# Performance work log

Measured on AMD Instinct MI355X. Metric: run time of the kernel, lower is better.

Reference implementation:

```python
import jax, jax.numpy as jnp
import numpy as np

HEADS = 8
NEG_SLOPE = 0.2  # PyG GATConv default negative_slope


def segment_softmax(logits, seg, num_segments):
    # logits: [E, H], seg: [E] destination ids
    m = jax.ops.segment_max(logits, seg, num_segments=num_segments)
    m = jnp.where(jnp.isfinite(m), m, 0.0)
    e = jnp.exp(logits - jax.lax.stop_gradient(m)[seg])
    s = jax.ops.segment_sum(e, seg, num_segments=num_segments)
    return e / (s[seg] + 1e-16)


def setup_inputs() -> dict:
    key = jax.random.key(0)
    k1, k2, k3, k4, k5, k6 = jax.random.split(key, 6)
    N, F_IN, H, C, E = 50000, 116, HEADS, 32, 800000
    x = jax.random.normal(k1, (N, F_IN), dtype=jnp.float32)
    edge_index = jax.random.randint(k2, (2, E), 0, N, dtype=jnp.int64)
    # Params (glorot-ish scale)
    W = jax.random.normal(k3, (F_IN, H * C), dtype=jnp.float32) * (1.0 / np.sqrt(F_IN))
    att_src = jax.random.normal(k4, (1, H, C), dtype=jnp.float32) * (1.0 / np.sqrt(C))
    att_dst = jax.random.normal(k5, (1, H, C), dtype=jnp.float32) * (1.0 / np.sqrt(C))
    bias = jnp.zeros((C,), dtype=jnp.float32)
    return {"x": x, "edge_index": edge_index, "W": W, "att_src": att_src, "att_dst": att_dst, "bias": bias}


def reference(x, edge_index, W, att_src, att_dst, bias):
    N = x.shape[0]
    H = HEADS
    C = W.shape[1] // H
    # Shared linear transform: [N, H, C]
    xt = (x @ W).reshape(N, H, C)
    alpha_src = jnp.sum(xt * att_src, axis=-1)  # [N, H]
    alpha_dst = jnp.sum(xt * att_dst, axis=-1)  # [N, H]
    # add_self_loops=True (PyG GATConv default)
    loops = jnp.arange(N, dtype=edge_index.dtype)
    src = jnp.concatenate([edge_index[0], loops])
    dst = jnp.concatenate([edge_index[1], loops])
    # Edge-wise attention logits + segment softmax over destination
    alpha = jax.nn.leaky_relu(alpha_src[src] + alpha_dst[dst], negative_slope=NEG_SLOPE)  # [E', H]
    alpha = segment_softmax(alpha, dst, N)
    # Weighted message aggregation
    msg = xt[src] * alpha[:, :, None]  # [E', H, C]
    out = jax.ops.segment_sum(msg, dst, num_segments=N)  # [N, H, C]
    # concat=False -> mean over heads, then bias
    out = out.mean(axis=1) + bias  # [N, C]
    return jax.nn.relu(out)
```

## Files before the change

### kernel.cpp

```cpp
#include <hip/hip_runtime.h>
#include <hip/hip_bf16.h>


#define F_IN 116
#define HC 256
#define NHEAD 8
#define CDIM 32
#define KP 128
#define ROWS_PB 48
#define DSLOT 64
#define ECHUNK 4096

typedef unsigned int uint32;
typedef short short8 __attribute__((ext_vector_type(8)));
typedef float f32x4 __attribute__((ext_vector_type(4)));

__device__ __forceinline__ unsigned short f2bf(float f) {
    uint32 u = __float_as_uint(f);
    u = (u + 0x7FFF + ((u >> 16) & 1)) >> 16;
    return (unsigned short)u;
}

__global__ void init_k(const float* __restrict__ W,
                       const float* __restrict__ att_s,
                       const float* __restrict__ att_d,
                       unsigned short* __restrict__ WbT,
                       unsigned short* __restrict__ WaT,
                       int* __restrict__ cnt, int N) {
    int idx = blockIdx.x * 256 + threadIdx.x;
    for (int i = idx; i < N; i += 144 * 256) cnt[i] = 0;
    if (idx < 32768) {
        int n = idx >> 7, k = idx & 127;
        WbT[idx] = (k < F_IN) ? f2bf(W[k * HC + n]) : (unsigned short)0;
    } else {
        int aid = idx - 32768;
        int col = aid >> 7, k = aid & 127;
        int tile = col >> 4;
        int cc = col & 15;
        int h = cc & 7, part = cc >> 3;
        const float* att = tile ? att_d : att_s;
        float s = 0.f;
        if (k < F_IN) {
            for (int c = 0; c < CDIM; ++c)
                s = fmaf(W[k * HC + h * CDIM + c], att[h * CDIM + c], s);
        }
        unsigned short hi = f2bf(s);
        unsigned short v = hi;
        if (part) {
            float rem = s - __uint_as_float((uint32)hi << 16);
            v = f2bf(rem);
        }
        WaT[col * KP + k] = v;
    }
}

__global__ __launch_bounds__(256) void fuse_k(const float* __restrict__ x,
                                              const unsigned short* __restrict__ WbT,
                                              const unsigned short* __restrict__ WaT,
                                              signed char* __restrict__ xq8,
                                              float* __restrict__ scl,
                                              float* __restrict__ asrc,
                                              float* __restrict__ adst,
                                              int N, int nScatGrp, int Ggemm,
                                              const int* __restrict__ src,
                                              const int* __restrict__ dst,
                                              int* __restrict__ cnt,
                                              unsigned short* __restrict__ csr, int E) {
    const int t = threadIdx.x;
    const int g = blockIdx.x >> 3, r = blockIdx.x & 7;
    const int c = g / 5, p = g - c * 5;

    if (p < 3) {
        const int sg = c * 3 + p;
        if (sg >= nScatGrp) return;
        const int sbid = sg * 8 + r;
        const int slice = sbid & 7;
        const int chunk = sbid >> 3;
        const int SLICE = (N + 7) >> 3;
        const int lo = slice * SLICE;
        const int hi = (lo + SLICE < N) ? lo + SLICE : N;
        const int ebase = chunk * ECHUNK + t * 4;
#pragma unroll
        for (int it = 0; it < ECHUNK / 1024; ++it) {
            int e = ebase + it * 1024;
            if (e < E) {
                int4 d4 = *(const int4*)&dst[e];
                int4 s4 = *(const int4*)&src[e];
                if (d4.x >= lo && d4.x < hi) {
                    int rr = atomicAdd(&cnt[d4.x], 1);
                    if (rr < DSLOT) csr[(d4.x << 6) + rr] = (unsigned short)s4.x;
                }
                if (d4.y >= lo && d4.y < hi) {
                    int rr = atomicAdd(&cnt[d4.y], 1);
                    if (rr < DSLOT) csr[(d4.y << 6) + rr] = (unsigned short)s4.y;
                }
                if (d4.z >= lo && d4.z < hi) {
                    int rr = atomicAdd(&cnt[d4.z], 1);
                    if (rr < DSLOT) csr[(d4.z << 6) + rr] = (unsigned short)s4.z;
                }
                if (d4.w >= lo && d4.w < hi) {
                    int rr = atomicAdd(&cnt[d4.w], 1);
                    if (rr < DSLOT) csr[(d4.w << 6) + rr] = (unsigned short)s4.w;
                }
            }
        }
        return;
    }

    const int gbid = (c * 2 + (p - 3)) * 8 + r;
    if (gbid >= Ggemm) return;

    __shared__ unsigned short xbs[16 * ROWS_PB * 8];
    const int row0 = gbid * ROWS_PB;
    for (int u = t; u < 16 * ROWS_PB; u += 256) {
        const int gg = u / ROWS_PB, rr = u - gg * ROWS_PB;
        const int gr = row0 + rr;
        f32x4 v0 = {0.f, 0.f, 0.f, 0.f}, v1 = {0.f, 0.f, 0.f, 0.f};
        if (gr < N) {
            const f32x4* xp = (const f32x4*)(x + (size_t)gr * F_IN + gg * 8);
            if (gg < 14) { v0 = xp[0]; v1 = xp[1]; }
            else if (gg == 14) { v0 = xp[0]; }
        }
        short8 pk;
        pk[0] = (short)f2bf(v0.x); pk[1] = (short)f2bf(v0.y);
        pk[2] = (short)f2bf(v0.z); pk[3] = (short)f2bf(v0.w);
        pk[4] = (short)f2bf(v1.x); pk[5] = (short)f2bf(v1.y);
        pk[6] = (short)f2bf(v1.z); pk[7] = (short)f2bf(v1.w);
        *(short8*)&xbs[u * 8] = pk;
    }
    __syncthreads();

    const int w = t >> 6, l = t & 63;
    const int q = l >> 4, m = l & 15;
    const int ncol0 = w * 64;

    short8 bfr[4][4];
#pragma unroll
    for (int nt = 0; nt < 4; ++nt)
#pragma unroll
        for (int ks = 0; ks < 4; ++ks)
            bfr[nt][ks] = *(const short8*)&WbT[(size_t)(ncol0 + nt * 16 + m) * KP + ks * 32 + q * 8];

    short8 wa[4];
    if (w < 2) {
#pragma unroll
        for (int ks = 0; ks < 4; ++ks)
            wa[ks] = *(const short8*)&WaT[(size_t)(w * 16 + m) * KP + ks * 32 + q * 8];
    }

    f32x4 acc[3][4];
#pragma unroll
    for (int rt = 0; rt < 3; ++rt)
#pragma unroll
        for (int nt = 0; nt < 4; ++nt) acc[rt][nt] = f32x4{0.f, 0.f, 0.f, 0.f};
    f32x4 acc_a[3];
#pragma unroll
    for (int rt = 0; rt < 3; ++rt) acc_a[rt] = f32x4{0.f, 0.f, 0.f, 0.f};

#pragma unroll
    for (int ks = 0; ks < 4; ++ks) {
        short8 a[3];
#pragma unroll
        for (int rt = 0; rt < 3; ++rt)
            a[rt] = *(const short8*)&xbs[((ks * 4 + q) * ROWS_PB + rt * 16 + m) * 8];
#pragma unroll
        for (int nt = 0; nt < 4; ++nt)
#pragma unroll
            for (int rt = 0; rt < 3; ++rt)
                acc[rt][nt] = __builtin_amdgcn_mfma_f32_16x16x32_bf16(bfr[nt][ks], a[rt], acc[rt][nt], 0, 0, 0);
        if (w < 2) {
#pragma unroll
            for (int rt = 0; rt < 3; ++rt)
                acc_a[rt] = __builtin_amdgcn_mfma_f32_16x16x32_bf16(wa[ks], a[rt], acc_a[rt], 0, 0, 0);
        }
    }

#pragma unroll
    for (int rt = 0; rt < 3; ++rt) {
        const int row = row0 + rt * 16 + m;
        float m0 = 0.f, m1 = 0.f;
#pragma unroll
        for (int rr = 0; rr < 4; ++rr) {
            m0 = fmaxf(m0, fmaxf(fabsf(acc[rt][0][rr]), fabsf(acc[rt][1][rr])));
            m1 = fmaxf(m1, fmaxf(fabsf(acc[rt][2][rr]), fabsf(acc[rt][3][rr])));
        }
        m0 = fmaxf(m0, __shfl_xor(m0, 16, 64));
        m0 = fmaxf(m0, __shfl_xor(m0, 32, 64));
        m1 = fmaxf(m1, __shfl_xor(m1, 16, 64));
        m1 = fmaxf(m1, __shfl_xor(m1, 32, 64));
        m0 = fmaxf(m0, 1e-20f);
        m1 = fmaxf(m1, 1e-20f);
        const float i0 = 127.f / m0, i1 = 127.f / m1;
        if (row < N) {
#pragma unroll
            for (int nt = 0; nt < 4; ++nt) {
                const float iv = (nt < 2) ? i0 : i1;
                uint32 pk = 0;
#pragma unroll
                for (int rr = 0; rr < 4; ++rr) {
                    int qv = __float2int_rn(acc[rt][nt][rr] * iv);
                    qv = (qv > 127) ? 127 : ((qv < -127) ? -127 : qv);
                    pk |= ((uint32)qv & 255u) << (8 * rr);
                }
                *(uint32*)&xq8[(size_t)row * HC + ncol0 + nt * 16 + q * 4] = pk;
            }
            if (q == 0) {
                float2 sc;
                sc.x = m0 * (1.f / 127.f);
                sc.y = m1 * (1.f / 127.f);
                *(float2*)&scl[row * NHEAD + 2 * w] = sc;
            }
        }
    }

    if (w < 2) {
        float* ap = (w == 0) ? asrc : adst;
#pragma unroll
        for (int rt = 0; rt < 3; ++rt) {
            f32x4 s;
#pragma unroll
            for (int rr = 0; rr < 4; ++rr) {
                float v = acc_a[rt][rr];
                s[rr] = v + __shfl_xor(v, 32, 64);
            }
            const int row = row0 + rt * 16 + m;
            if (q < 2 && row < N)
                *(f32x4*)&ap[row * NHEAD + q * 4] = s;
        }
    }
}

__global__ __launch_bounds__(256) void aggregate_k(const signed char* __restrict__ xq8,
                                                   const float* __restrict__ scl,
                                                   const float* __restrict__ asrc,
                                                   const float* __restrict__ adst,
                                                   const int* __restrict__ cnt,
                                                   const unsigned short* __restrict__ csr,
                                                   const float* __restrict__ bias,
                                                   float* __restrict__ out, int N) {
    const int t = threadIdx.x;
    const int lg = t & 31;
    const int base = t & 32;
    const int n = blockIdx.x * 8 + (t >> 5);
    if (n >= N) return;

    const int h_f = lg >> 2;
    const int h_w = lg & 7;
    const int e_w = lg >> 3;

    const int beg = n << 6;
    int d = cnt[n];
    if (d > DSLOT) d = DSLOT;

    const float adst_hw = adst[n * NHEAD + h_w];

    float zs = asrc[n * NHEAD + h_f] + adst[n * NHEAD + h_f];
    zs = (zs > 0.f) ? zs : 0.2f * zs;
    const float wself = __expf(zs);
    const float wselfs = wself * scl[n * NHEAD + h_f];

    uint2 sv = ((const uint2*)(xq8 + (size_t)n * HC))[lg];
    float a0 = wselfs * (float)((int)(sv.x << 24) >> 24);
    float a1 = wselfs * (float)((int)(sv.x << 16) >> 24);
    float a2 = wselfs * (float)((int)(sv.x <<  8) >> 24);
    float a3 = wselfs * (float)((int)sv.x         >> 24);
    float a4 = wselfs * (float)((int)(sv.y << 24) >> 24);
    float a5 = wselfs * (float)((int)(sv.y << 16) >> 24);
    float a6 = wselfs * (float)((int)(sv.y <<  8) >> 24);
    float a7 = wselfs * (float)((int)sv.y         >> 24);
    float wsum = wself;

    const int nfull = d >> 2;
    const int rem = d & 3;
    int pos = beg;
    for (int cch = 0; cch < nfull; ++cch, pos += 4) {
        int s_w = (int)csr[pos + e_w];
        float z = asrc[s_w * NHEAD + h_w] + adst_hw;
        z = (z > 0.f) ? z : 0.2f * z;
        float w_reg = __expf(z);
        float wsc_reg = w_reg * scl[s_w * NHEAD + h_w];
#pragma unroll
        for (int e = 0; e < 4; ++e) {
            int s = __shfl(s_w, base + (e << 3), 64);
            float w  = __shfl(w_reg,  base + (e << 3) + h_f, 64);
            float ws = __shfl(wsc_reg, base + (e << 3) + h_f, 64);
            uint2 v = ((const uint2*)(xq8 + (size_t)s * HC))[lg];
            a0 = fmaf(ws, (float)((int)(v.x << 24) >> 24), a0);
            a1 = fmaf(ws, (float)((int)(v.x << 16) >> 24), a1);
            a2 = fmaf(ws, (float)((int)(v.x <<  8) >> 24), a2);
            a3 = fmaf(ws, (float)((int)v.x         >> 24), a3);
            a4 = fmaf(ws, (float)((int)(v.y << 24) >> 24), a4);
            a5 = fmaf(ws, (float)((int)(v.y << 16) >> 24), a5);
            a6 = fmaf(ws, (float)((int)(v.y <<  8) >> 24), a6);
            a7 = fmaf(ws, (float)((int)v.y         >> 24), a7);
            wsum += w;
        }
    }
    if (rem) {
        int s_w = (e_w < rem) ? (int)csr[pos + e_w] : n;
        float z = asrc[s_w * NHEAD + h_w] + adst_hw;
        z = (z > 0.f) ? z : 0.2f * z;
        float w_reg = __expf(z);
        float wsc_reg = w_reg * scl[s_w * NHEAD + h_w];
        for (int e = 0; e < rem; ++e) {
            int s = __shfl(s_w, base + (e << 3), 64);
            float w  = __shfl(w_reg,  base + (e << 3) + h_f, 64);
            float ws = __shfl(wsc_reg, base + (e << 3) + h_f, 64);
            uint2 v = ((const uint2*)(xq8 + (size_t)s * HC))[lg];
            a0 = fmaf(ws, (float)((int)(v.x << 24) >> 24), a0);
            a1 = fmaf(ws, (float)((int)(v.x << 16) >> 24), a1);
            a2 = fmaf(ws, (float)((int)(v.x <<  8) >> 24), a2);
            a3 = fmaf(ws, (float)((int)v.x         >> 24), a3);
            a4 = fmaf(ws, (float)((int)(v.y << 24) >> 24), a4);
            a5 = fmaf(ws, (float)((int)(v.y << 16) >> 24), a5);
            a6 = fmaf(ws, (float)((int)(v.y <<  8) >> 24), a6);
            a7 = fmaf(ws, (float)((int)v.y         >> 24), a7);
            wsum += w;
        }
    }

    const float inv = 1.f / (wsum + 1e-16f);
    a0 *= inv; a1 *= inv; a2 *= inv; a3 *= inv;
    a4 *= inv; a5 *= inv; a6 *= inv; a7 *= inv;

#pragma unroll
    for (int o = 4; o <= 16; o <<= 1) {
        a0 += __shfl_xor(a0, o, 64);
        a1 += __shfl_xor(a1, o, 64);
        a2 += __shfl_xor(a2, o, 64);
        a3 += __shfl_xor(a3, o, 64);
        a4 += __shfl_xor(a4, o, 64);
        a5 += __shfl_xor(a5, o, 64);
        a6 += __shfl_xor(a6, o, 64);
        a7 += __shfl_xor(a7, o, 64);
    }

    if (lg < 4) {
        const float* bp = bias + 8 * lg;
        float4 r0, r1;
        r0.x = fmaxf(a0 * 0.125f + bp[0], 0.f);
        r0.y = fmaxf(a1 * 0.125f + bp[1], 0.f);
        r0.z = fmaxf(a2 * 0.125f + bp[2], 0.f);
        r0.w = fmaxf(a3 * 0.125f + bp[3], 0.f);
        r1.x = fmaxf(a4 * 0.125f + bp[4], 0.f);
        r1.y = fmaxf(a5 * 0.125f + bp[5], 0.f);
        r1.z = fmaxf(a6 * 0.125f + bp[6], 0.f);
        r1.w = fmaxf(a7 * 0.125f + bp[7], 0.f);
        *(float4*)&out[(size_t)n * CDIM + 8 * lg] = r0;
        *(float4*)&out[(size_t)n * CDIM + 8 * lg + 4] = r1;
    }
}

extern "C" void kernel_launch(void* const* d_in, const int* in_sizes, int n_in,
                              void* d_out, int out_size, void* d_ws, size_t ws_size,
                              hipStream_t stream) {
    const float* x     = (const float*)d_in[0];
    const int*   ei    = (const int*)d_in[1];
    const float* W     = (const float*)d_in[2];
    const float* att_s = (const float*)d_in[3];
    const float* att_d = (const float*)d_in[4];
    const float* bias  = (const float*)d_in[5];
    float* out = (float*)d_out;

    const int N = in_sizes[0] / F_IN;
    const int E = in_sizes[1] / 2;

    signed char* xq8 = (signed char*)d_ws;
    float* scl = (float*)((char*)d_ws + (size_t)N * HC);
    unsigned short* WbT = (unsigned short*)((char*)d_ws + (size_t)2 * N * HC);
    float* asrc = (float*)(WbT + 256 * KP);
    float* adst = asrc + (size_t)N * NHEAD;
    int*   cnt  = (int*)(adst + (size_t)N * NHEAD);
    unsigned short* csr = (unsigned short*)(cnt + N);
    unsigned short* WaT = csr + (size_t)N * DSLOT;

    const int Ggemm = (N + ROWS_PB - 1) / ROWS_PB;
    const int nchunk = (E + ECHUNK - 1) / ECHUNK;
    const int Gscat = nchunk * 8;
    const int nScatGrp = (Gscat + 7) / 8;
    const int nGemmGrp = (Ggemm + 7) / 8;
    const int cS = (nScatGrp + 2) / 3;
    const int cG = (nGemmGrp + 1) / 2;
    const int ncyc = (cS > cG) ? cS : cG;
    const int Gfuse = ncyc * 5 * 8;

    init_k<<<144, 256, 0, stream>>>(W, att_s, att_d, WbT, WaT, cnt, N);
    fuse_k<<<Gfuse, 256, 0, stream>>>(x, WbT, WaT, xq8, scl, asrc, adst,
                                      N, nScatGrp, Ggemm,
                                      ei, ei + E, cnt, csr, E);
    aggregate_k<<<(N + 7) / 8, 256, 0, stream>>>(xq8, scl, asrc, adst, cnt, csr, bias, out, N);
}
```

Measured before the change: 182.4 us.

## Merge init, scatter/GEMM and aggregation into one cooperative persistent kernel

Replaces the three separate kernel launches with a single cooperative kernel whose grid is sized from occupancy and CU count. Stages are separated by grid-wide syncs, and the blocks loop persistently over scatter chunks, GEMM tiles and aggregation node groups. Odd and even blocks alternate the order of scatter and GEMM so the two overlap. This removes launch gaps and the inter-kernel drain, but adds two grid barriers, per-call host queries (occupancy, device properties), and a smaller grid that may reduce latency hiding in the gather-heavy aggregation.

```diff
diff --git a/kernel.cpp b/kernel.cpp
--- a/kernel.cpp
+++ b/kernel.cpp
@@ -1,5 +1,6 @@
 #include <hip/hip_runtime.h>
 #include <hip/hip_bf16.h>
+#include <hip/hip_cooperative_groups.h>
 
 
 #define F_IN 116
@@ -15,339 +16,341 @@
 typedef short short8 __attribute__((ext_vector_type(8)));
 typedef float f32x4 __attribute__((ext_vector_type(4)));
 
+namespace cg = cooperative_groups;
+
 __device__ __forceinline__ unsigned short f2bf(float f) {
     uint32 u = __float_as_uint(f);
     u = (u + 0x7FFF + ((u >> 16) & 1)) >> 16;
     return (unsigned short)u;
 }
 
-__global__ void init_k(const float* __restrict__ W,
-                       const float* __restrict__ att_s,
-                       const float* __restrict__ att_d,
-                       unsigned short* __restrict__ WbT,
-                       unsigned short* __restrict__ WaT,
-                       int* __restrict__ cnt, int N) {
-    int idx = blockIdx.x * 256 + threadIdx.x;
-    for (int i = idx; i < N; i += 144 * 256) cnt[i] = 0;
-    if (idx < 32768) {
-        int n = idx >> 7, k = idx & 127;
-        WbT[idx] = (k < F_IN) ? f2bf(W[k * HC + n]) : (unsigned short)0;
-    } else {
-        int aid = idx - 32768;
-        int col = aid >> 7, k = aid & 127;
-        int tile = col >> 4;
-        int cc = col & 15;
-        int h = cc & 7, part = cc >> 3;
-        const float* att = tile ? att_d : att_s;
-        float s = 0.f;
-        if (k < F_IN) {
-            for (int c = 0; c < CDIM; ++c)
-                s = fmaf(W[k * HC + h * CDIM + c], att[h * CDIM + c], s);
-        }
-        unsigned short hi = f2bf(s);
-        unsigned short v = hi;
-        if (part) {
-            float rem = s - __uint_as_float((uint32)hi << 16);
-            v = f2bf(rem);
-        }
-        WaT[col * KP + k] = v;
+__global__ __launch_bounds__(256) void gat_k(
+        const float* __restrict__ x,
+        const int* __restrict__ src,
+        const int* __restrict__ dst,
+        const float* __restrict__ W,
+        const float* __restrict__ att_s,
+        const float* __restrict__ att_d,
+        const float* __restrict__ bias,
+        unsigned short* __restrict__ WbT,
+        unsigned short* __restrict__ WaT,
+        signed char* __restrict__ xq8,
+        float* __restrict__ scl,
+        float* __restrict__ asrc,
+        float* __restrict__ adst,
+        int* __restrict__ cnt,
+        unsigned short* __restrict__ csr,
+        float* __restrict__ out,
+        int N, int E, int nchunk, int Ggemm, int NG) {
+    const int t = threadIdx.x;
+    const int b = blockIdx.x;
+    const int G = gridDim.x;
+    __shared__ unsigned short xbs[16 * ROWS_PB * 8];
+
+    for (int i = b * 256 + t; i < N; i += G * 256) cnt[i] = 0;
+    for (int idx = b * 256 + t; idx < 36864; idx += G * 256) {
+        if (idx < 32768) {
+            int n = idx >> 7, k = idx & 127;
+            WbT[idx] = (k < F_IN) ? f2bf(W[k * HC + n]) : (unsigned short)0;
+        } else {
+            int aid = idx - 32768;
+            int col = aid >> 7, k = aid & 127;
+            int tile = col >> 4;
+            int cc = col & 15;
+            int h = cc & 7, part = cc >> 3;
+            const float* att = tile ? att_d : att_s;
+            float s = 0.f;
+            if (k < F_IN) {
+                for (int c = 0; c < CDIM; ++c)
+                    s = fmaf(W[k * HC + h * CDIM + c], att[h * CDIM + c], s);
+            }
+            unsigned short hi = f2bf(s);
+            unsigned short v = hi;
+            if (part) {
+                float rem = s - __uint_as_float((uint32)hi << 16);
+                v = f2bf(rem);
+            }
+            WaT[col * KP + k] = v;
+        }
     }
-}
-
-__global__ __launch_bounds__(256) void fuse_k(const float* __restrict__ x,
-                                              const unsigned short* __restrict__ WbT,
-                                              const unsigned short* __restrict__ WaT,
-                                              signed char* __restrict__ xq8,
-                                              float* __restrict__ scl,
-                                              float* __restrict__ asrc,
-                                              float* __restrict__ adst,
-                                              int N, int nScatGrp, int Ggemm,
-                                              const int* __restrict__ src,
-                                              const int* __restrict__ dst,
-                                              int* __restrict__ cnt,
-                                              unsigned short* __restrict__ csr, int E) {
-    const int t = threadIdx.x;
-    const int g = blockIdx.x >> 3, r = blockIdx.x & 7;
-    const int c = g / 5, p = g - c * 5;
-
-    if (p < 3) {
-        const int sg = c * 3 + p;
-        if (sg >= nScatGrp) return;
-        const int sbid = sg * 8 + r;
-        const int slice = sbid & 7;
-        const int chunk = sbid >> 3;
+    cg::this_grid().sync();
+
+    auto do_scatter = [&]() {
+        const int slice = b & 7;
         const int SLICE = (N + 7) >> 3;
         const int lo = slice * SLICE;
         const int hi = (lo + SLICE < N) ? lo + SLICE : N;
-        const int ebase = chunk * ECHUNK + t * 4;
-#pragma unroll
-        for (int it = 0; it < ECHUNK / 1024; ++it) {
-            int e = ebase + it * 1024;
-            if (e < E) {
-                int4 d4 = *(const int4*)&dst[e];
-                int4 s4 = *(const int4*)&src[e];
-                if (d4.x >= lo && d4.x < hi) {
-                    int rr = atomicAdd(&cnt[d4.x], 1);
-                    if (rr < DSLOT) csr[(d4.x << 6) + rr] = (unsigned short)s4.x;
-                }
-                if (d4.y >= lo && d4.y < hi) {
-                    int rr = atomicAdd(&cnt[d4.y], 1);
-                    if (rr < DSLOT) csr[(d4.y << 6) + rr] = (unsigned short)s4.y;
-                }
-                if (d4.z >= lo && d4.z < hi) {
-                    int rr = atomicAdd(&cnt[d4.z], 1);
-                    if (rr < DSLOT) csr[(d4.z << 6) + rr] = (unsigned short)s4.z;
-                }
-                if (d4.w >= lo && d4.w < hi) {
-                    int rr = atomicAdd(&cnt[d4.w], 1);
-                    if (rr < DSLOT) csr[(d4.w << 6) + rr] = (unsigned short)s4.w;
-                }
-            }
-        }
-        return;
-    }
-
-    const int gbid = (c * 2 + (p - 3)) * 8 + r;
-    if (gbid >= Ggemm) return;
-
-    __shared__ unsigned short xbs[16 * ROWS_PB * 8];
-    const int row0 = gbid * ROWS_PB;
-    for (int u = t; u < 16 * ROWS_PB; u += 256) {
-        const int gg = u / ROWS_PB, rr = u - gg * ROWS_PB;
-        const int gr = row0 + rr;
-        f32x4 v0 = {0.f, 0.f, 0.f, 0.f}, v1 = {0.f, 0.f, 0.f, 0.f};
-        if (gr < N) {
-            const f32x4* xp = (const f32x4*)(x + (size_t)gr * F_IN + gg * 8);
-            if (gg < 14) { v0 = xp[0]; v1 = xp[1]; }
-            else if (gg == 14) { v0 = xp[0]; }
-        }
-        short8 pk;
-        pk[0] = (short)f2bf(v0.x); pk[1] = (short)f2bf(v0.y);
-        pk[2] = (short)f2bf(v0.z); pk[3] = (short)f2bf(v0.w);
-        pk[4] = (short)f2bf(v1.x); pk[5] = (short)f2bf(v1.y);
-        pk[6] = (short)f2bf(v1.z); pk[7] = (short)f2bf(v1.w);
-        *(short8*)&xbs[u * 8] = pk;
-    }
-    __syncthreads();
-
-    const int w = t >> 6, l = t & 63;
-    const int q = l >> 4, m = l & 15;
-    const int ncol0 = w * 64;
-
-    short8 bfr[4][4];
-#pragma unroll
-    for (int nt = 0; nt < 4; ++nt)
-#pragma unroll
-        for (int ks = 0; ks < 4; ++ks)
-            bfr[nt][ks] = *(const short8*)&WbT[(size_t)(ncol0 + nt * 16 + m) * KP + ks * 32 + q * 8];
-
-    short8 wa[4];
-    if (w < 2) {
-#pragma unroll
-        for (int ks = 0; ks < 4; ++ks)
-            wa[ks] = *(const short8*)&WaT[(size_t)(w * 16 + m) * KP + ks * 32 + q * 8];
-    }
-
-    f32x4 acc[3][4];
-#pragma unroll
-    for (int rt = 0; rt < 3; ++rt)
-#pragma unroll
-        for (int nt = 0; nt < 4; ++nt) acc[rt][nt] = f32x4{0.f, 0.f, 0.f, 0.f};
-    f32x4 acc_a[3];
-#pragma unroll
-    for (int rt = 0; rt < 3; ++rt) acc_a[rt] = f32x4{0.f, 0.f, 0.f, 0.f};
-
-#pragma unroll
-    for (int ks = 0; ks < 4; ++ks) {
-        short8 a[3];
-#pragma unroll
-        for (int rt = 0; rt < 3; ++rt)
-            a[rt] = *(const short8*)&xbs[((ks * 4 + q) * ROWS_PB + rt * 16 + m) * 8];
-#pragma unroll
-        for (int nt = 0; nt < 4; ++nt)
+        const int Gs = G >> 3;
+        for (int c = b >> 3; c < nchunk; c += Gs) {
+            const int ebase = c * ECHUNK + t * 4;
+#pragma unroll
+            for (int it = 0; it < ECHUNK / 1024; ++it) {
+                int e = ebase + it * 1024;
+                if (e < E) {
+                    int4 d4 = *(const int4*)&dst[e];
+                    int4 s4 = *(const int4*)&src[e];
+                    if (d4.x >= lo && d4.x < hi) {
+                        int rr = atomicAdd(&cnt[d4.x], 1);
+                        if (rr < DSLOT) csr[(d4.x << 6) + rr] = (unsigned short)s4.x;
+                    }
+                    if (d4.y >= lo && d4.y < hi) {
+                        int rr = atomicAdd(&cnt[d4.y], 1);
+                        if (rr < DSLOT) csr[(d4.y << 6) + rr] = (unsigned short)s4.y;
+                    }
+                    if (d4.z >= lo && d4.z < hi) {
+                        int rr = atomicAdd(&cnt[d4.z], 1);
+                        if (rr < DSLOT) csr[(d4.z << 6) + rr] = (unsigned short)s4.z;
+                    }
+                    if (d4.w >= lo && d4.w < hi) {
+                        int rr = atomicAdd(&cnt[d4.w], 1);
+                        if (rr < DSLOT) csr[(d4.w << 6) + rr] = (unsigned short)s4.w;
+                    }
+                }
+            }
+        }
+    };
+
+    auto do_gemm = [&]() {
+        for (int g2 = b; g2 < Ggemm; g2 += G) {
+            __syncthreads();
+            const int row0 = g2 * ROWS_PB;
+            for (int u = t; u < 16 * ROWS_PB; u += 256) {
+                const int gg = u / ROWS_PB, rr = u - gg * ROWS_PB;
+                const int gr = row0 + rr;
+                f32x4 v0 = {0.f, 0.f, 0.f, 0.f}, v1 = {0.f, 0.f, 0.f, 0.f};
+                if (gr < N) {
+                    const f32x4* xp = (const f32x4*)(x + (size_t)gr * F_IN + gg * 8);
+                    if (gg < 14) { v0 = xp[0]; v1 = xp[1]; }
+                    else if (gg == 14) { v0 = xp[0]; }
+                }
+                short8 pk;
+                pk[0] = (short)f2bf(v0.x); pk[1] = (short)f2bf(v0.y);
+                pk[2] = (short)f2bf(v0.z); pk[3] = (short)f2bf(v0.w);
+                pk[4] = (short)f2bf(v1.x); pk[5] = (short)f2bf(v1.y);
+                pk[6] = (short)f2bf(v1.z); pk[7] = (short)f2bf(v1.w);
+                *(short8*)&xbs[u * 8] = pk;
+            }
+            __syncthreads();
+
+            const int w = t >> 6, l = t & 63;
+            const int q = l >> 4, m = l & 15;
+            const int ncol0 = w * 64;
+
+            short8 bfr[4][4];
+#pragma unroll
+            for (int nt = 0; nt < 4; ++nt)
+#pragma unroll
+                for (int ks = 0; ks < 4; ++ks)
+                    bfr[nt][ks] = *(const short8*)&WbT[(size_t)(ncol0 + nt * 16 + m) * KP + ks * 32 + q * 8];
+
+            short8 wa[4];
+            if (w < 2) {
+#pragma unroll
+                for (int ks = 0; ks < 4; ++ks)
+                    wa[ks] = *(const short8*)&WaT[(size_t)(w * 16 + m) * KP + ks * 32 + q * 8];
+            }
+
+            f32x4 acc[3][4];
 #pragma unroll
             for (int rt = 0; rt < 3; ++rt)
-                acc[rt][nt] = __builtin_amdgcn_mfma_f32_16x16x32_bf16(bfr[nt][ks], a[rt], acc[rt][nt], 0, 0, 0);
-        if (w < 2) {
-#pragma unroll
-            for (int rt = 0; rt < 3; ++rt)
-                acc_a[rt] = __builtin_amdgcn_mfma_f32_16x16x32_bf16(wa[ks], a[rt], acc_a[rt], 0, 0, 0);
-        }
-    }
-
-#pragma unroll
-    for (int rt = 0; rt < 3; ++rt) {
-        const int row = row0 + rt * 16 + m;
-        float m0 = 0.f, m1 = 0.f;
-#pragma unroll
-        for (int rr = 0; rr < 4; ++rr) {
-            m0 = fmaxf(m0, fmaxf(fabsf(acc[rt][0][rr]), fabsf(acc[rt][1][rr])));
-            m1 = fmaxf(m1, fmaxf(fabsf(acc[rt][2][rr]), fabsf(acc[rt][3][rr])));
-        }
-        m0 = fmaxf(m0, __shfl_xor(m0, 16, 64));
-        m0 = fmaxf(m0, __shfl_xor(m0, 32, 64));
-        m1 = fmaxf(m1, __shfl_xor(m1, 16, 64));
-        m1 = fmaxf(m1, __shfl_xor(m1, 32, 64));
-        m0 = fmaxf(m0, 1e-20f);
-        m1 = fmaxf(m1, 1e-20f);
-        const float i0 = 127.f / m0, i1 = 127.f / m1;
-        if (row < N) {
-#pragma unroll
-            for (int nt = 0; nt < 4; ++nt) {
-                const float iv = (nt < 2) ? i0 : i1;
-                uint32 pk = 0;
+#pragma unroll
+                for (int nt = 0; nt < 4; ++nt) acc[rt][nt] = f32x4{0.f, 0.f, 0.f, 0.f};
+            f32x4 acc_a[3];
+#pragma unroll
+            for (int rt = 0; rt < 3; ++rt) acc_a[rt] = f32x4{0.f, 0.f, 0.f, 0.f};
+
+#pragma unroll
+            for (int ks = 0; ks < 4; ++ks) {
+                short8 a[3];
+#pragma unroll
+                for (int rt = 0; rt < 3; ++rt)
+                    a[rt] = *(const short8*)&xbs[((ks * 4 + q) * ROWS_PB + rt * 16 + m) * 8];
+#pragma unroll
+                for (int nt = 0; nt < 4; ++nt)
+#pragma unroll
+                    for (int rt = 0; rt < 3; ++rt)
+                        acc[rt][nt] = __builtin_amdgcn_mfma_f32_16x16x32_bf16(bfr[nt][ks], a[rt], acc[rt][nt], 0, 0, 0);
+                if (w < 2) {
+#pragma unroll
+                    for (int rt = 0; rt < 3; ++rt)
+                        acc_a[rt] = __builtin_amdgcn_mfma_f32_16x16x32_bf16(wa[ks], a[rt], acc_a[rt], 0, 0, 0);
+                }
+            }
+
+#pragma unroll
+            for (int rt = 0; rt < 3; ++rt) {
+                const int row = row0 + rt * 16 + m;
+                float m0 = 0.f, m1 = 0.f;
 #pragma unroll
                 for (int rr = 0; rr < 4; ++rr) {
-                    int qv = __float2int_rn(acc[rt][nt][rr] * iv);
-                    qv = (qv > 127) ? 127 : ((qv < -127) ? -127 : qv);
-                    pk |= ((uint32)qv & 255u) << (8 * rr);
-                }
-                *(uint32*)&xq8[(size_t)row * HC + ncol0 + nt * 16 + q * 4] = pk;
-            }
-            if (q == 0) {
-                float2 sc;
-                sc.x = m0 * (1.f / 127.f);
-                sc.y = m1 * (1.f / 127.f);
-                *(float2*)&scl[row * NHEAD + 2 * w] = sc;
-            }
-        }
-    }
-
-    if (w < 2) {
-        float* ap = (w == 0) ? asrc : adst;
-#pragma unroll
-        for (int rt = 0; rt < 3; ++rt) {
-            f32x4 s;
-#pragma unroll
-            for (int rr = 0; rr < 4; ++rr) {
-                float v = acc_a[rt][rr];
-                s[rr] = v + __shfl_xor(v, 32, 64);
-            }
-            const int row = row0 + rt * 16 + m;
-            if (q < 2 && row < N)
-                *(f32x4*)&ap[row * NHEAD + q * 4] = s;
-        }
-    }
-}
-
-__global__ __launch_bounds__(256) void aggregate_k(const signed char* __restrict__ xq8,
-                                                   const float* __restrict__ scl,
-                                                   const float* __restrict__ asrc,
-                                                   const float* __restrict__ adst,
-                                                   const int* __restrict__ cnt,
-                                                   const unsigned short* __restrict__ csr,
-                                                   const float* __restrict__ bias,
-                                                   float* __restrict__ out, int N) {
-    const int t = threadIdx.x;
-    const int lg = t & 31;
-    const int base = t & 32;
-    const int n = blockIdx.x * 8 + (t >> 5);
-    if (n >= N) return;
-
-    const int h_f = lg >> 2;
-    const int h_w = lg & 7;
-    const int e_w = lg >> 3;
-
-    const int beg = n << 6;
-    int d = cnt[n];
-    if (d > DSLOT) d = DSLOT;
-
-    const float adst_hw = adst[n * NHEAD + h_w];
-
-    float zs = asrc[n * NHEAD + h_f] + adst[n * NHEAD + h_f];
-    zs = (zs > 0.f) ? zs : 0.2f * zs;
-    const float wself = __expf(zs);
-    const float wselfs = wself * scl[n * NHEAD + h_f];
-
-    uint2 sv = ((const uint2*)(xq8 + (size_t)n * HC))[lg];
-    float a0 = wselfs * (float)((int)(sv.x << 24) >> 24);
-    float a1 = wselfs * (float)((int)(sv.x << 16) >> 24);
-    float a2 = wselfs * (float)((int)(sv.x <<  8) >> 24);
-    float a3 = wselfs * (float)((int)sv.x         >> 24);
-    float a4 = wselfs * (float)((int)(sv.y << 24) >> 24);
-    float a5 = wselfs * (float)((int)(sv.y << 16) >> 24);
-    float a6 = wselfs * (float)((int)(sv.y <<  8) >> 24);
-    float a7 = wselfs * (float)((int)sv.y         >> 24);
-    float wsum = wself;
-
-    const int nfull = d >> 2;
-    const int rem = d & 3;
-    int pos = beg;
-    for (int cch = 0; cch < nfull; ++cch, pos += 4) {
-        int s_w = (int)csr[pos + e_w];
-        float z = asrc[s_w * NHEAD + h_w] + adst_hw;
-        z = (z > 0.f) ? z : 0.2f * z;
-        float w_reg = __expf(z);
-        float wsc_reg = w_reg * scl[s_w * NHEAD + h_w];
-#pragma unroll
-        for (int e = 0; e < 4; ++e) {
-            int s = __shfl(s_w, base + (e << 3), 64);
-            float w  = __shfl(w_reg,  base + (e << 3) + h_f, 64);
-            float ws = __shfl(wsc_reg, base + (e << 3) + h_f, 64);
-            uint2 v = ((const uint2*)(xq8 + (size_t)s * HC))[lg];
-            a0 = fmaf(ws, (float)((int)(v.x << 24) >> 24), a0);
-            a1 = fmaf(ws, (float)((int)(v.x << 16) >> 24), a1);
-            a2 = fmaf(ws, (float)((int)(v.x <<  8) >> 24), a2);
-            a3 = fmaf(ws, (float)((int)v.x         >> 24), a3);
-            a4 = fmaf(ws, (float)((int)(v.y << 24) >> 24), a4);
-            a5 = fmaf(ws, (float)((int)(v.y << 16) >> 24), a5);
-            a6 = fmaf(ws, (float)((int)(v.y <<  8) >> 24), a6);
-            a7 = fmaf(ws, (float)((int)v.y         >> 24), a7);
-            wsum += w;
-        }
-    }
-    if (rem) {
-        int s_w = (e_w < rem) ? (int)csr[pos + e_w] : n;
-        float z = asrc[s_w * NHEAD + h_w] + adst_hw;
-        z = (z > 0.f) ? z : 0.2f * z;
-        float w_reg = __expf(z);
-        float wsc_reg = w_reg * scl[s_w * NHEAD + h_w];
-        for (int e = 0; e < rem; ++e) {
-            int s = __shfl(s_w, base + (e << 3), 64);
-            float w  = __shfl(w_reg,  base + (e << 3) + h_f, 64);
-            float ws = __shfl(wsc_reg, base + (e << 3) + h_f, 64);
-            uint2 v = ((const uint2*)(xq8 + (size_t)s * HC))[lg];
-            a0 = fmaf(ws, (float)((int)(v.x << 24) >> 24), a0);
-            a1 = fmaf(ws, (float)((int)(v.x << 16) >> 24), a1);
-            a2 = fmaf(ws, (float)((int)(v.x <<  8) >> 24), a2);
-            a3 = fmaf(ws, (float)((int)v.x         >> 24), a3);
-            a4 = fmaf(ws, (float)((int)(v.y << 24) >> 24), a4);
-            a5 = fmaf(ws, (float)((int)(v.y << 16) >> 24), a5);
-            a6 = fmaf(ws, (float)((int)(v.y <<  8) >> 24), a6);
-            a7 = fmaf(ws, (float)((int)v.y         >> 24), a7);
-            wsum += w;
-        }
-    }
-
-    const float inv = 1.f / (wsum + 1e-16f);
-    a0 *= inv; a1 *= inv; a2 *= inv; a3 *= inv;
-    a4 *= inv; a5 *= inv; a6 *= inv; a7 *= inv;
-
-#pragma unroll
-    for (int o = 4; o <= 16; o <<= 1) {
-        a0 += __shfl_xor(a0, o, 64);
-        a1 += __shfl_xor(a1, o, 64);
-        a2 += __shfl_xor(a2, o, 64);
-        a3 += __shfl_xor(a3, o, 64);
-        a4 += __shfl_xor(a4, o, 64);
-        a5 += __shfl_xor(a5, o, 64);
-        a6 += __shfl_xor(a6, o, 64);
-        a7 += __shfl_xor(a7, o, 64);
-    }
-
-    if (lg < 4) {
-        const float* bp = bias + 8 * lg;
-        float4 r0, r1;
-        r0.x = fmaxf(a0 * 0.125f + bp[0], 0.f);
-        r0.y = fmaxf(a1 * 0.125f + bp[1], 0.f);
-        r0.z = fmaxf(a2 * 0.125f + bp[2], 0.f);
-        r0.w = fmaxf(a3 * 0.125f + bp[3], 0.f);
-        r1.x = fmaxf(a4 * 0.125f + bp[4], 0.f);
-        r1.y = fmaxf(a5 * 0.125f + bp[5], 0.f);
-        r1.z = fmaxf(a6 * 0.125f + bp[6], 0.f);
-        r1.w = fmaxf(a7 * 0.125f + bp[7], 0.f);
-        *(float4*)&out[(size_t)n * CDIM + 8 * lg] = r0;
-        *(float4*)&out[(size_t)n * CDIM + 8 * lg + 4] = r1;
+                    m0 = fmaxf(m0, fmaxf(fabsf(acc[rt][0][rr]), fabsf(acc[rt][1][rr])));
+                    m1 = fmaxf(m1, fmaxf(fabsf(acc[rt][2][rr]), fabsf(acc[rt][3][rr])));
+                }
+                m0 = fmaxf(m0, __shfl_xor(m0, 16, 64));
+                m0 = fmaxf(m0, __shfl_xor(m0, 32, 64));
+                m1 = fmaxf(m1, __shfl_xor(m1, 16, 64));
+                m1 = fmaxf(m1, __shfl_xor(m1, 32, 64));
+                m0 = fmaxf(m0, 1e-20f);
+                m1 = fmaxf(m1, 1e-20f);
+                const float i0 = 127.f / m0, i1 = 127.f / m1;
+                if (row < N) {
+#pragma unroll
+                    for (int nt = 0; nt < 4; ++nt) {
+                        const float iv = (nt < 2) ? i0 : i1;
+                        uint32 pk = 0;
+#pragma unroll
+                        for (int rr = 0; rr < 4; ++rr) {
+                            int qv = __float2int_rn(acc[rt][nt][rr] * iv);
+                            qv = (qv > 127) ? 127 : ((qv < -127) ? -127 : qv);
+                            pk |= ((uint32)qv & 255u) << (8 * rr);
+                        }
+                        *(uint32*)&xq8[(size_t)row * HC + ncol0 + nt * 16 + q * 4] = pk;
+                    }
+                    if (q == 0) {
+                        float2 sc;
+                        sc.x = m0 * (1.f / 127.f);
+                        sc.y = m1 * (1.f / 127.f);
+                        *(float2*)&scl[row * NHEAD + 2 * w] = sc;
+                    }
+                }
+            }
+
+            if (w < 2) {
+                float* ap = (w == 0) ? asrc : adst;
+#pragma unroll
+                for (int rt = 0; rt < 3; ++rt) {
+                    f32x4 s;
+#pragma unroll
+                    for (int rr = 0; rr < 4; ++rr) {
+                        float v = acc_a[rt][rr];
+                        s[rr] = v + __shfl_xor(v, 32, 64);
+                    }
+                    const int row = row0 + rt * 16 + m;
+                    if (q < 2 && row < N)
+                        *(f32x4*)&ap[row * NHEAD + q * 4] = s;
+                }
+            }
+        }
+    };
+
+    if (b & 1) { do_gemm(); do_scatter(); }
+    else       { do_scatter(); do_gemm(); }
+
+    cg::this_grid().sync();
+
+    for (int ng = b; ng < NG; ng += G) {
+        const int lg = t & 31;
+        const int base = t & 32;
+        const int n = ng * 8 + (t >> 5);
+        if (n >= N) continue;
+
+        const int h_f = lg >> 2;
+        const int h_w = lg & 7;
+        const int e_w = lg >> 3;
+
+        const int beg = n << 6;
+        int d;
+        if (lg == 0) d = atomicAdd(&cnt[n], 0);
+        d = __shfl(d, base, 64);
+        if (d > DSLOT) d = DSLOT;
+
+        const float adst_hw = adst[n * NHEAD + h_w];
+
+        float zs = asrc[n * NHEAD + h_f] + adst[n * NHEAD + h_f];
+        zs = (zs > 0.f) ? zs : 0.2f * zs;
+        const float wself = __expf(zs);
+        const float wselfs = wself * scl[n * NHEAD + h_f];
+
+        uint2 sv = ((const uint2*)(xq8 + (size_t)n * HC))[lg];
+        float a0 = wselfs * (float)((int)(sv.x << 24) >> 24);
+        float a1 = wselfs * (float)((int)(sv.x << 16) >> 24);
+        float a2 = wselfs * (float)((int)(sv.x <<  8) >> 24);
+        float a3 = wselfs * (float)((int)sv.x         >> 24);
+        float a4 = wselfs * (float)((int)(sv.y << 24) >> 24);
+        float a5 = wselfs * (float)((int)(sv.y << 16) >> 24);
+        float a6 = wselfs * (float)((int)(sv.y <<  8) >> 24);
+        float a7 = wselfs * (float)((int)sv.y         >> 24);
+        float wsum = wself;
+
+        const int nfull = d >> 2;
+        const int rem = d & 3;
+        int pos = beg;
+        for (int cch = 0; cch < nfull; ++cch, pos += 4) {
+            int s_w = (int)csr[pos + e_w];
+            float z = asrc[s_w * NHEAD + h_w] + adst_hw;
+            z = (z > 0.f) ? z : 0.2f * z;
+            float w_reg = __expf(z);
+            float wsc_reg = w_reg * scl[s_w * NHEAD + h_w];
+#pragma unroll
+            for (int e = 0; e < 4; ++e) {
+                int s = __shfl(s_w, base + (e << 3), 64);
+                float w  = __shfl(w_reg,  base + (e << 3) + h_f, 64);
+                float ws = __shfl(wsc_reg, base + (e << 3) + h_f, 64);
+                uint2 v = ((const uint2*)(xq8 + (size_t)s * HC))[lg];
+                a0 = fmaf(ws, (float)((int)(v.x << 24) >> 24), a0);
+                a1 = fmaf(ws, (float)((int)(v.x << 16) >> 24), a1);
+                a2 = fmaf(ws, (float)((int)(v.x <<  8) >> 24), a2);
+                a3 = fmaf(ws, (float)((int)v.x         >> 24), a3);
+                a4 = fmaf(ws, (float)((int)(v.y << 24) >> 24), a4);
+                a5 = fmaf(ws, (float)((int)(v.y << 16) >> 24), a5);
+                a6 = fmaf(ws, (float)((int)(v.y <<  8) >> 24), a6);
+                a7 = fmaf(ws, (float)((int)v.y         >> 24), a7);
+                wsum += w;
+            }
+        }
+        if (rem) {
+            int s_w = (e_w < rem) ? (int)csr[pos + e_w] : n;
+            float z = asrc[s_w * NHEAD + h_w] + adst_hw;
+            z = (z > 0.f) ? z : 0.2f * z;
+            float w_reg = __expf(z);
+            float wsc_reg = w_reg * scl[s_w * NHEAD + h_w];
+            for (int e = 0; e < rem; ++e) {
+                int s = __shfl(s_w, base + (e << 3), 64);
+                float w  = __shfl(w_reg,  base + (e << 3) + h_f, 64);
+                float ws = __shfl(wsc_reg, base + (e << 3) + h_f, 64);
+                uint2 v = ((const uint2*)(xq8 + (size_t)s * HC))[lg];
+                a0 = fmaf(ws, (float)((int)(v.x << 24) >> 24), a0);
+                a1 = fmaf(ws, (float)((int)(v.x << 16) >> 24), a1);
+                a2 = fmaf(ws, (float)((int)(v.x <<  8) >> 24), a2);
+                a3 = fmaf(ws, (float)((int)v.x         >> 24), a3);
+                a4 = fmaf(ws, (float)((int)(v.y << 24) >> 24), a4);
+                a5 = fmaf(ws, (float)((int)(v.y << 16) >> 24), a5);
+                a6 = fmaf(ws, (float)((int)(v.y <<  8) >> 24), a6);
+                a7 = fmaf(ws, (float)((int)v.y         >> 24), a7);
+                wsum += w;
+            }
+        }
+
+        const float inv = 1.f / (wsum + 1e-16f);
+        a0 *= inv; a1 *= inv; a2 *= inv; a3 *= inv;
+        a4 *= inv; a5 *= inv; a6 *= inv; a7 *= inv;
+
+#pragma unroll
+        for (int o = 4; o <= 16; o <<= 1) {
+            a0 += __shfl_xor(a0, o, 64);
+            a1 += __shfl_xor(a1, o, 64);
+            a2 += __shfl_xor(a2, o, 64);
+            a3 += __shfl_xor(a3, o, 64);
+            a4 += __shfl_xor(a4, o, 64);
+            a5 += __shfl_xor(a5, o, 64);
+            a6 += __shfl_xor(a6, o, 64);
+            a7 += __shfl_xor(a7, o, 64);
+        }
+
+        if (lg < 4) {
+            const float* bp = bias + 8 * lg;
+            float4 r0, r1;
+            r0.x = fmaxf(a0 * 0.125f + bp[0], 0.f);
+            r0.y = fmaxf(a1 * 0.125f + bp[1], 0.f);
+            r0.z = fmaxf(a2 * 0.125f + bp[2], 0.f);
+            r0.w = fmaxf(a3 * 0.125f + bp[3], 0.f);
+            r1.x = fmaxf(a4 * 0.125f + bp[4], 0.f);
+            r1.y = fmaxf(a5 * 0.125f + bp[5], 0.f);
+            r1.z = fmaxf(a6 * 0.125f + bp[6], 0.f);
+            r1.w = fmaxf(a7 * 0.125f + bp[7], 0.f);
+            *(float4*)&out[(size_t)n * CDIM + 8 * lg] = r0;
+            *(float4*)&out[(size_t)n * CDIM + 8 * lg + 4] = r1;
+        }
     }
 }
 
@@ -362,8 +365,8 @@
     const float* bias  = (const float*)d_in[5];
     float* out = (float*)d_out;
 
-    const int N = in_sizes[0] / F_IN;
-    const int E = in_sizes[1] / 2;
+    int N = in_sizes[0] / F_IN;
+    int E = in_sizes[1] / 2;
 
     signed char* xq8 = (signed char*)d_ws;
     float* scl = (float*)((char*)d_ws + (size_t)N * HC);
@@ -374,19 +377,33 @@
     unsigned short* csr = (unsigned short*)(cnt + N);
     unsigned short* WaT = csr + (size_t)N * DSLOT;
 
-    const int Ggemm = (N + ROWS_PB - 1) / ROWS_PB;
-    const int nchunk = (E + ECHUNK - 1) / ECHUNK;
-    const int Gscat = nchunk * 8;
-    const int nScatGrp = (Gscat + 7) / 8;
-    const int nGemmGrp = (Ggemm + 7) / 8;
-    const int cS = (nScatGrp + 2) / 3;
-    const int cG = (nGemmGrp + 1) / 2;
-    const int ncyc = (cS > cG) ? cS : cG;
-    const int Gfuse = ncyc * 5 * 8;
-
-    init_k<<<144, 256, 0, stream>>>(W, att_s, att_d, WbT, WaT, cnt, N);
-    fuse_k<<<Gfuse, 256, 0, stream>>>(x, WbT, WaT, xq8, scl, asrc, adst,
-                                      N, nScatGrp, Ggemm,
-                                      ei, ei + E, cnt, csr, E);
-    aggregate_k<<<(N + 7) / 8, 256, 0, stream>>>(xq8, scl, asrc, adst, cnt, csr, bias, out, N);
+    int Ggemm  = (N + ROWS_PB - 1) / ROWS_PB;
+    int nchunk = (E + ECHUNK - 1) / ECHUNK;
+    int NG     = (N + 7) / 8;
+
+    const int* src_p = ei;
+    const int* dst_p = ei + E;
+
+    int occ = 0;
+    (void)hipOccupancyMaxActiveBlocksPerMultiprocessor(
+        &occ, reinterpret_cast<const void*>(gat_k), 256, 0);
+    if (occ < 1) occ = 1;
+    int nCU = 256;
+    hipDeviceProp_t prop;
+    if (hipGetDeviceProperties(&prop, 0) == hipSuccess && prop.multiProcessorCount > 0)
+        nCU = prop.multiProcessorCount;
+    long long Gl = (long long)occ * nCU;
+    int G = (Gl > 2048) ? 2048 : (int)Gl;
+    G &= ~7;
+    if (G < 8) G = 8;
+
+    void* args[] = {
+        (void*)&x, (void*)&src_p, (void*)&dst_p, (void*)&W, (void*)&att_s,
+        (void*)&att_d, (void*)&bias, (void*)&WbT, (void*)&WaT, (void*)&xq8,
+        (void*)&scl, (void*)&asrc, (void*)&adst, (void*)&cnt, (void*)&csr,
+        (void*)&out, (void*)&N, (void*)&E, (void*)&nchunk, (void*)&Ggemm,
+        (void*)&NG
+    };
+    (void)hipLaunchCooperativeKernel(reinterpret_cast<const void*>(gat_k),
+                                     dim3(G), dim3(256), args, 0, stream);
 }
```

After: 382.3 us. +109.6%, slower.

## Scatter each edge once instead of slicing destinations across eight blocks

Applied to the files above, without the earlier changes.

The CSR build used to have eight blocks read every edge chunk, each keeping only the destinations in its own node slice. Now each block handles a distinct 1024-edge range and issues all four atomics directly, removing the repeated edge reads. The block interleave between scatter and GEMM work is also rebalanced from groups of eight to a flat 3:4 pattern per cycle. This gives up the per-XCD destination locality the slicing provided, so atomics and CSR writes may spread across caches.

```diff
diff --git a/kernel.cpp b/kernel.cpp
--- a/kernel.cpp
+++ b/kernel.cpp
@@ -9,7 +9,6 @@
 #define KP 128
 #define ROWS_PB 48
 #define DSLOT 64
-#define ECHUNK 4096
 
 typedef unsigned int uint32;
 typedef short short8 __attribute__((ext_vector_type(8)));
@@ -61,53 +60,34 @@
                                               float* __restrict__ scl,
                                               float* __restrict__ asrc,
                                               float* __restrict__ adst,
-                                              int N, int nScatGrp, int Ggemm,
+                                              int N, int nScat, int Ggemm,
                                               const int* __restrict__ src,
                                               const int* __restrict__ dst,
                                               int* __restrict__ cnt,
                                               unsigned short* __restrict__ csr, int E) {
     const int t = threadIdx.x;
-    const int g = blockIdx.x >> 3, r = blockIdx.x & 7;
-    const int c = g / 5, p = g - c * 5;
+    const int c = blockIdx.x / 7, p = blockIdx.x - c * 7;
 
     if (p < 3) {
-        const int sg = c * 3 + p;
-        if (sg >= nScatGrp) return;
-        const int sbid = sg * 8 + r;
-        const int slice = sbid & 7;
-        const int chunk = sbid >> 3;
-        const int SLICE = (N + 7) >> 3;
-        const int lo = slice * SLICE;
-        const int hi = (lo + SLICE < N) ? lo + SLICE : N;
-        const int ebase = chunk * ECHUNK + t * 4;
-#pragma unroll
-        for (int it = 0; it < ECHUNK / 1024; ++it) {
-            int e = ebase + it * 1024;
-            if (e < E) {
-                int4 d4 = *(const int4*)&dst[e];
-                int4 s4 = *(const int4*)&src[e];
-                if (d4.x >= lo && d4.x < hi) {
-                    int rr = atomicAdd(&cnt[d4.x], 1);
-                    if (rr < DSLOT) csr[(d4.x << 6) + rr] = (unsigned short)s4.x;
-                }
-                if (d4.y >= lo && d4.y < hi) {
-                    int rr = atomicAdd(&cnt[d4.y], 1);
-                    if (rr < DSLOT) csr[(d4.y << 6) + rr] = (unsigned short)s4.y;
-                }
-                if (d4.z >= lo && d4.z < hi) {
-                    int rr = atomicAdd(&cnt[d4.z], 1);
-                    if (rr < DSLOT) csr[(d4.z << 6) + rr] = (unsigned short)s4.z;
-                }
-                if (d4.w >= lo && d4.w < hi) {
-                    int rr = atomicAdd(&cnt[d4.w], 1);
-                    if (rr < DSLOT) csr[(d4.w << 6) + rr] = (unsigned short)s4.w;
-                }
-            }
+        const int sbid = c * 3 + p;
+        if (sbid >= nScat) return;
+        const int e = sbid * 1024 + t * 4;
+        if (e < E) {
+            int4 d4 = *(const int4*)&dst[e];
+            int4 s4 = *(const int4*)&src[e];
+            int r0 = atomicAdd(&cnt[d4.x], 1);
+            int r1 = atomicAdd(&cnt[d4.y], 1);
+            int r2 = atomicAdd(&cnt[d4.z], 1);
+            int r3 = atomicAdd(&cnt[d4.w], 1);
+            if (r0 < DSLOT) csr[(d4.x << 6) + r0] = (unsigned short)s4.x;
+            if (r1 < DSLOT) csr[(d4.y << 6) + r1] = (unsigned short)s4.y;
+            if (r2 < DSLOT) csr[(d4.z << 6) + r2] = (unsigned short)s4.z;
+            if (r3 < DSLOT) csr[(d4.w << 6) + r3] = (unsigned short)s4.w;
         }
         return;
     }
 
-    const int gbid = (c * 2 + (p - 3)) * 8 + r;
+    const int gbid = c * 4 + (p - 3);
     if (gbid >= Ggemm) return;
 
     __shared__ unsigned short xbs[16 * ROWS_PB * 8];
@@ -375,18 +355,15 @@
     unsigned short* WaT = csr + (size_t)N * DSLOT;
 
     const int Ggemm = (N + ROWS_PB - 1) / ROWS_PB;
-    const int nchunk = (E + ECHUNK - 1) / ECHUNK;
-    const int Gscat = nchunk * 8;
-    const int nScatGrp = (Gscat + 7) / 8;
-    const int nGemmGrp = (Ggemm + 7) / 8;
-    const int cS = (nScatGrp + 2) / 3;
-    const int cG = (nGemmGrp + 1) / 2;
+    const int nScat = (E + 1023) / 1024;
+    const int cS = (nScat + 2) / 3;
+    const int cG = (Ggemm + 3) / 4;
     const int ncyc = (cS > cG) ? cS : cG;
-    const int Gfuse = ncyc * 5 * 8;
+    const int Gfuse = ncyc * 7;
 
     init_k<<<144, 256, 0, stream>>>(W, att_s, att_d, WbT, WaT, cnt, N);
     fuse_k<<<Gfuse, 256, 0, stream>>>(x, WbT, WaT, xq8, scl, asrc, adst,
-                                      N, nScatGrp, Ggemm,
+                                      N, nScat, Ggemm,
                                       ei, ei + E, cnt, csr, E);
     aggregate_k<<<(N + 7) / 8, 256, 0, stream>>>(xq8, scl, asrc, adst, cnt, csr, bias, out, N);
 }
```

Result: faster. 169.7 us (median of 2 runs) (-7.0%).
